# Kernel tuning notes

Hardware: AMD Instinct MI355X
Metric: run time of the kernel (lower is better)

## Reference

```python
import jax, jax.numpy as jnp
import numpy as np

N = 32768      # total nodes
E = 262144     # total edges (avg degree 8)
S = 128        # graph segments
B = 16         # batch entries
C = S // B     # segments per batch entry
NF, NC = 90, 36
OP, OD = 120, 64
D0, DX, GIN, GH = 190, 380, 256, 512


def setup_inputs() -> dict:
    key = jax.random.key(0)
    ks = jax.random.split(key, 16)
    rn = lambda k, shape, s=0.02: jax.random.normal(k, shape, jnp.float32) * s
    return {
        "node_features": jax.random.normal(ks[0], (N, NF), jnp.float32),
        "node_config_features": jax.random.normal(ks[1], (N, NC), jnp.float32),
        "emb_table": rn(ks[2], (OP, OD), 1.0),
        "w1": rn(ks[3], (DX, D0)), "b1": jnp.zeros((DX,), jnp.float32),
        "g1": jnp.ones((DX,), jnp.float32), "be1": jnp.zeros((DX,), jnp.float32),
        "w2": rn(ks[4], (GIN, DX)), "b2": jnp.zeros((GIN,), jnp.float32),
        "g2": jnp.ones((GIN,), jnp.float32), "be2": jnp.zeros((GIN,), jnp.float32),
        "wl1": rn(ks[5], (GH, GIN)), "bl1": jnp.zeros((GH,), jnp.float32), "wr1": rn(ks[6], (GH, GIN)),
        "wl2": rn(ks[7], (GH, GH)), "bl2": jnp.zeros((GH,), jnp.float32), "wr2": rn(ks[8], (GH, GH)),
        "wl3": rn(ks[9], (GH, GH)), "bl3": jnp.zeros((GH,), jnp.float32), "wr3": rn(ks[10], (GH, GH)),
        "wc": rn(ks[11], (1, GH)), "bc": jnp.zeros((1,), jnp.float32),
        "node_ops": jax.random.randint(ks[12], (N,), 0, OP),
        "edges": jax.random.randint(ks[13], (2, E), 0, N),
        # cumulative end indices, equal-size segments; batches = segment -> batch entry
        "node_separation": (jnp.arange(S, dtype=jnp.int32) + 1) * (N // S),
        "batches": jnp.repeat(jnp.arange(B, dtype=jnp.int32), C),
    }


def _leaky(x):
    return jnp.where(x >= 0, x, 0.01 * x)


def _graphwise_ln(x, seg_id, counts, gamma, beta):
    # per-graph-segment mean/var over all nodes and features, per-feature affine
    D = x.shape[1]
    s = jax.ops.segment_sum(jnp.sum(x, -1), seg_id, num_segments=S)
    ss = jax.ops.segment_sum(jnp.sum(x * x, -1), seg_id, num_segments=S)
    cnt = counts.astype(x.dtype) * D
    mean = s / cnt
    var = ss / cnt - mean * mean
    inv = jax.lax.rsqrt(var + 1e-5)
    return (x - mean[seg_id, None]) * inv[seg_id, None] * gamma + beta


def _pairnorm(x):
    # PyG PairNorm, scale=1: center over nodes, divide by sqrt(mean row norm^2)
    xc = x - jnp.mean(x, axis=0, keepdims=True)
    denom = 1e-5 + jnp.sqrt(jnp.mean(jnp.sum(xc * xc, -1)))
    return xc / denom


def _sage(x, src, dst, inv_deg, wl, bl, wr):
    # SAGEConv(mean): lin_l(mean_neighbors) + lin_r(x)
    agg = jax.ops.segment_sum(x[src], dst, num_segments=N) * inv_deg[:, None]
    return agg @ wl.T + bl + x @ wr.T


def reference(node_features, node_config_features, emb_table, w1, b1, g1, be1,
              w2, b2, g2, be2, wl1, bl1, wr1, wl2, bl2, wr2, wl3, bl3, wr3,
              wc, bc, node_ops, edges, node_separation, batches):
    seg_id = jnp.searchsorted(node_separation, jnp.arange(N), side="right")
    counts = jnp.diff(node_separation, prepend=0)
    src, dst = edges[0], edges[1]
    deg = jax.ops.segment_sum(jnp.ones((E,), jnp.float32), dst, num_segments=N)
    inv_deg = 1.0 / jnp.maximum(deg, 1.0)

    x = jnp.concatenate([node_features, node_config_features, emb_table[node_ops]], axis=1)
    # node_features_mlp: Linear -> LeakyReLU -> GLN -> Linear -> LeakyReLU -> GLN
    x = _graphwise_ln(_leaky(x @ w1.T + b1), seg_id, counts, g1, be1)
    x = _graphwise_ln(_leaky(x @ w2.T + b2), seg_id, counts, g2, be2)
    # GraphSAGE: 3 layers, PairNorm + ReLU after all but the last
    x = jax.nn.relu(_pairnorm(_sage(x, src, dst, inv_deg, wl1, bl1, wr1)))
    x = jax.nn.relu(_pairnorm(_sage(x, src, dst, inv_deg, wl2, bl2, wr2)))
    x = _sage(x, src, dst, inv_deg, wl3, bl3, wr3)
    # ragged per-segment sum pooling (replaces the python loop) -> [S, GH]
    seg_sums = jax.ops.segment_sum(x, seg_id, num_segments=S)
    # batches = repeat(arange(B), C) and segments are in order -> reshape groups
    agg = seg_sums.reshape(B, C, GH)
    out = agg @ wc.T + bc  # [B, C, 1]
    return jnp.squeeze(out, 2)
```

## Files before the change

kernel.cpp:

```cpp
#include <hip/hip_runtime.h>
#include <hip/hip_bf16.h>

#define NN   32768
#define EE   262144
#define SS   128
#define NF_  90
#define NC_  36
#define OD_  64
#define D0_  190
#define DX_  380
#define GIN_ 256
#define GH_  512

typedef __attribute__((ext_vector_type(8))) short  s8v;
typedef __attribute__((ext_vector_type(4))) float  f4v;

typedef const __attribute__((address_space(1))) void* gas_ptr;
typedef __attribute__((address_space(3))) void*       las_ptr;

__device__ __forceinline__ float bf2f(unsigned u) {
  return __uint_as_float(u << 16);
}
__device__ __forceinline__ unsigned short f2bf(float f) {
  unsigned u = __float_as_uint(f);
  u += 0x7FFFu + ((u >> 16) & 1u);
  return (unsigned short)(u >> 16);
}
__device__ __forceinline__ unsigned pack2(float a, float b) {
  return ((unsigned)f2bf(b) << 16) | (unsigned)f2bf(a);
}

__global__ void deg_count(const int* __restrict__ dst, int* __restrict__ deg) {
  int e = blockIdx.x * 256 + threadIdx.x;
  if (e < EE) atomicAdd(&deg[dst[e]], 1);
}

__global__ __launch_bounds__(256) void blk_sum_k(const int* __restrict__ deg,
                                                 int* __restrict__ bsum) {
  __shared__ int buf[256];
  int tid = threadIdx.x;
  buf[tid] = deg[blockIdx.x * 256 + tid];
  __syncthreads();
  for (int off = 128; off > 0; off >>= 1) {
    if (tid < off) buf[tid] += buf[tid + off];
    __syncthreads();
  }
  if (tid == 0) bsum[blockIdx.x] = buf[0];
}

__global__ __launch_bounds__(128) void blk_scan_k(const int* __restrict__ bsum,
                                                  int* __restrict__ boff) {
  __shared__ int buf[128];
  int tid = threadIdx.x;
  int v = bsum[tid];
  buf[tid] = v;
  __syncthreads();
  for (int d = 1; d < 128; d <<= 1) {
    int t = (tid >= d) ? buf[tid - d] : 0;
    __syncthreads();
    if (tid >= d) buf[tid] += t;
    __syncthreads();
  }
  boff[tid] = buf[tid] - v;
}

__global__ __launch_bounds__(256) void offsets_k(const int* __restrict__ deg,
                                                 const int* __restrict__ boff,
                                                 int* __restrict__ offsets,
                                                 float* __restrict__ inv_deg) {
  __shared__ int buf[256];
  int tid = threadIdx.x;
  int i = blockIdx.x * 256 + tid;
  int v = deg[i];
  buf[tid] = v;
  __syncthreads();
  for (int d = 1; d < 256; d <<= 1) {
    int t = (tid >= d) ? buf[tid - d] : 0;
    __syncthreads();
    if (tid >= d) buf[tid] += t;
    __syncthreads();
  }
  offsets[i] = boff[blockIdx.x] + buf[tid] - v;
  inv_deg[i] = 1.0f / fmaxf((float)v, 1.0f);
  if (i == 0) offsets[NN] = EE;
}

__global__ void bucket_k(const int* __restrict__ src, const int* __restrict__ dst,
                         const int* __restrict__ offsets, int* __restrict__ cursor,
                         int* __restrict__ srcs) {
  int e = blockIdx.x * 256 + threadIdx.x;
  if (e < EE) {
    int d = dst[e];
    int pos = offsets[d] + atomicAdd(&cursor[d], 1);
    srcs[pos] = src[e];
  }
}

#define CW1  73728
#define CW2  172032
#define CWL1 303104
#define CWR1 434176
#define CWL2 696320
#define CWR2 958464
#define CWL3 1220608
#define CWR3 1482752

__global__ __launch_bounds__(256) void prep_all(
    const float* __restrict__ nf, const float* __restrict__ ncf,
    const float* __restrict__ emb, const int* __restrict__ ops,
    const float* __restrict__ w1, const float* __restrict__ w2,
    const float* __restrict__ wl1, const float* __restrict__ wr1,
    const float* __restrict__ wl2, const float* __restrict__ wr2,
    const float* __restrict__ wl3, const float* __restrict__ wr3,
    unsigned short* __restrict__ w1b, unsigned short* __restrict__ w2b,
    unsigned short* __restrict__ wl1b, unsigned short* __restrict__ wr1b,
    unsigned short* __restrict__ wl2b, unsigned short* __restrict__ wr2b,
    unsigned short* __restrict__ wl3b, unsigned short* __restrict__ wr3b,
    unsigned short* __restrict__ x0,
    float* __restrict__ stat_all, float* __restrict__ outp,
    const float* __restrict__ bc)
{
  const int T = 4096 * 256;
  int gidx = blockIdx.x * 256 + threadIdx.x;
  for (int i = gidx; i < 2560; i += T) stat_all[i] = 0.0f;
  if (gidx < SS) outp[gidx] = bc[0];
  for (int i = gidx; i < CWR3; i += T) {
    if (i < CW1) {
      int r = i / 192, c = i - r * 192;
      w1b[i] = f2bf((r < DX_ && c < D0_) ? w1[r * D0_ + c] : 0.0f);
    } else if (i < CW2) {
      int j = i - CW1;
      int r = j / 384, c = j - r * 384;
      w2b[j] = f2bf((c < DX_) ? w2[r * DX_ + c] : 0.0f);
    } else if (i < CWL1) { int j = i - CW2;  wl1b[j] = f2bf(wl1[j]); }
    else if (i < CWR1)   { int j = i - CWL1; wr1b[j] = f2bf(wr1[j]); }
    else if (i < CWL2)   { int j = i - CWR1; wl2b[j] = f2bf(wl2[j]); }
    else if (i < CWR2)   { int j = i - CWL2; wr2b[j] = f2bf(wr2[j]); }
    else if (i < CWL3)   { int j = i - CWR2; wl3b[j] = f2bf(wl3[j]); }
    else                 { int j = i - CWL3; wr3b[j] = f2bf(wr3[j]); }
  }
  for (int i = gidx; i < NN * 192; i += T) {
    int n = i / 192;
    int c = i - n * 192;
    float v;
    if (c < NF_)            v = nf[n * NF_ + c];
    else if (c < NF_ + NC_) v = ncf[n * NC_ + (c - NF_)];
    else if (c < D0_)       v = emb[ops[n] * OD_ + (c - (NF_ + NC_))];
    else                    v = 0.0f;
    x0[i] = f2bf(v);
  }
}

__device__ __forceinline__ void stage_tile_async(const unsigned short* __restrict__ G, int ld,
                                                 int base_row, int k0,
                                                 unsigned short* __restrict__ lds, int tid) {
#pragma unroll
  for (int i = 0; i < 2; ++i) {
    int c = tid + i * 256;
    int row = c & 127;
    int off = c >> 7;
    const unsigned short* src = G + (size_t)(base_row + row) * ld + k0 + off * 8;
    unsigned short* dst = lds + off * 1024 + row * 8;
    __builtin_amdgcn_global_load_lds((gas_ptr)(const void*)src, (las_ptr)(void*)dst,
                                     16, 0, 0);
  }
}

__global__ __launch_bounds__(256) void mfma_gemm2(
    const unsigned short* __restrict__ A1, int lda1,
    const unsigned short* __restrict__ B1, int ldb1, int K1,
    const unsigned short* __restrict__ A2, int lda2,
    const unsigned short* __restrict__ B2, int ldb2, int K2,
    const float* __restrict__ bias,
    float* __restrict__ C, int ldc, int Nreal, int mode, int swz,
    float* __restrict__ st0, float* __restrict__ st1,
    const float* __restrict__ wcp, float* __restrict__ outp)
{
  __shared__ unsigned short As[4096];
  __shared__ unsigned short Bs[4096];
  int tid = threadIdx.x;
  int lane = tid & 63;
  int w = tid >> 6;
  int wm = (w & 1) * 64;
  int wn = (w >> 1) * 64;
  int bm, bn;
  if (swz) {
    int L = blockIdx.x;
    int xcd = L & 7;
    int s = L >> 3;
    bn = (s & 3) * 128;
    bm = ((s >> 2) * 8 + xcd) * 128;
  } else {
    bm = blockIdx.y * 128;
    bn = blockIdx.x * 128;
  }
  int quad = lane >> 4;
  int r16 = lane & 15;

  f4v acc[4][4] = {};

#pragma unroll 1
  for (int ph = 0; ph < 2; ++ph) {
    const unsigned short* A = ph ? A2 : A1;
    const unsigned short* B = ph ? B2 : B1;
    int lda = ph ? lda2 : lda1;
    int ldb = ph ? ldb2 : ldb1;
    int K = ph ? K2 : K1;
    for (int k0 = 0; k0 < K; k0 += 32) {
      stage_tile_async(A, lda, bm, k0, As, tid);
      stage_tile_async(B, ldb, bn, k0, Bs, tid);
      __syncthreads();
      s8v af[4], bfr[4];
#pragma unroll
      for (int mi = 0; mi < 4; ++mi)
        af[mi] = *(const s8v*)&As[quad * 1024 + (wm + mi * 16 + r16) * 8];
#pragma unroll
      for (int ni = 0; ni < 4; ++ni)
        bfr[ni] = *(const s8v*)&Bs[quad * 1024 + (wn + ni * 16 + r16) * 8];
#pragma unroll
      for (int mi = 0; mi < 4; ++mi)
#pragma unroll
        for (int ni = 0; ni < 4; ++ni)
          acc[mi][ni] = __builtin_amdgcn_mfma_f32_16x16x32_bf16(
              af[mi], bfr[ni], acc[mi][ni], 0, 0, 0);
      __syncthreads();
    }
  }

  float* red = (float*)As;
  float* cs  = (float*)Bs;
  float* css = ((float*)Bs) + 128;

  int seg = bm >> 8;

  if (mode == 1) {
    float lsum = 0.0f, lssq = 0.0f;
#pragma unroll
    for (int mi = 0; mi < 4; ++mi) {
      int gm = bm + wm + mi * 16 + quad * 4;
#pragma unroll
      for (int ni = 0; ni < 4; ++ni) {
        int gn = bn + wn + ni * 16 + r16;
        if (gn < Nreal) {
          float bv = bias[gn];
#pragma unroll
          for (int r = 0; r < 4; ++r) {
            float v = acc[mi][ni][r] + bv;
            v = (v >= 0.0f) ? v : 0.01f * v;
            C[(size_t)(gm + r) * ldc + gn] = v;
            lsum += v;
            lssq += v * v;
          }
        }
      }
    }
    red[tid] = lsum;
    __syncthreads();
    for (int off = 128; off > 0; off >>= 1) {
      if (tid < off) red[tid] += red[tid + off];
      __syncthreads();
    }
    if (tid == 0) atomicAdd(&st0[seg], red[0]);
    __syncthreads();
    red[tid] = lssq;
    __syncthreads();
    for (int off = 128; off > 0; off >>= 1) {
      if (tid < off) red[tid] += red[tid + off];
      __syncthreads();
    }
    if (tid == 0) atomicAdd(&st1[seg], red[0]);
  } else if (mode == 2) {
    if (tid < 128) { cs[tid] = 0.0f; css[tid] = 0.0f; }
    __syncthreads();
#pragma unroll
    for (int ni = 0; ni < 4; ++ni) {
      int col = wn + ni * 16 + r16;
      int gn = bn + col;
      float bv = bias[gn];
      float psum = 0.0f, pssq = 0.0f;
#pragma unroll
      for (int mi = 0; mi < 4; ++mi) {
        int gm = bm + wm + mi * 16 + quad * 4;
#pragma unroll
        for (int r = 0; r < 4; ++r) {
          float v = acc[mi][ni][r] + bv;
          C[(size_t)(gm + r) * ldc + gn] = v;
          psum += v;
          pssq += v * v;
        }
      }
      atomicAdd(&cs[col], psum);
      atomicAdd(&css[col], pssq);
    }
    __syncthreads();
    if (tid < 128) {
      atomicAdd(&st0[bn + tid], cs[tid]);
      atomicAdd(&st1[bn + tid], css[tid]);
    }
  } else {
    float part = 0.0f;
#pragma unroll
    for (int ni = 0; ni < 4; ++ni) {
      int gn = bn + wn + ni * 16 + r16;
      float bv = bias[gn];
      float wv = wcp[gn];
      float colsum = 0.0f;
#pragma unroll
      for (int mi = 0; mi < 4; ++mi)
#pragma unroll
        for (int r = 0; r < 4; ++r)
          colsum += acc[mi][ni][r] + bv;
      part += colsum * wv;
    }
    red[tid] = part;
    __syncthreads();
    for (int off = 128; off > 0; off >>= 1) {
      if (tid < off) red[tid] += red[tid + off];
      __syncthreads();
    }
    if (tid == 0) atomicAdd(&outp[seg], red[0]);
  }
}

__global__ __launch_bounds__(256) void gln_apply_bf16(
    const float* __restrict__ x, int ld, int D, int Dp,
    const float* __restrict__ seg_sum, const float* __restrict__ seg_ssq,
    const float* __restrict__ g, const float* __restrict__ be,
    unsigned short* __restrict__ out) {
  int r = blockIdx.x;
  int s = r >> 8;
  float cnt = 256.0f * (float)D;
  float m = seg_sum[s] / cnt;
  float var = seg_ssq[s] / cnt - m * m;
  float inv = rsqrtf(var + 1e-5f);
  const float* row = x + (size_t)r * ld;
  unsigned short* orow = out + (size_t)r * Dp;
  for (int c = threadIdx.x; c < Dp; c += 256) {
    float v = (c < D) ? ((row[c] - m) * inv * g[c] + be[c]) : 0.0f;
    orow[c] = f2bf(v);
  }
}

__global__ __launch_bounds__(256) void aggregate8(const unsigned short* __restrict__ x,
                                                  int L8,
                                                  unsigned short* __restrict__ agg,
                                                  const int* __restrict__ offsets,
                                                  const int* __restrict__ srcs,
                                                  const float* __restrict__ inv_deg) {
  int tid = threadIdx.x;
  int n = (blockIdx.x << (8 - L8)) + (tid >> L8);
  int f8 = tid & ((1 << L8) - 1);
  int start = offsets[n], end = offsets[n + 1];
  float wgt = inv_deg[n];
  const uint4* xb = (const uint4*)x;
  float a0 = 0, a1 = 0, a2 = 0, a3 = 0, a4 = 0, a5 = 0, a6 = 0, a7 = 0;
  for (int e = start; e < end; ++e) {
    uint4 v = xb[((size_t)srcs[e] << L8) + f8];
    a0 += bf2f(v.x & 0xffffu); a1 += bf2f(v.x >> 16);
    a2 += bf2f(v.y & 0xffffu); a3 += bf2f(v.y >> 16);
    a4 += bf2f(v.z & 0xffffu); a5 += bf2f(v.z >> 16);
    a6 += bf2f(v.w & 0xffffu); a7 += bf2f(v.w >> 16);
  }
  uint4 o;
  o.x = pack2(a0 * wgt, a1 * wgt);
  o.y = pack2(a2 * wgt, a3 * wgt);
  o.z = pack2(a4 * wgt, a5 * wgt);
  o.w = pack2(a6 * wgt, a7 * wgt);
  ((uint4*)agg)[((size_t)n << L8) + f8] = o;
}

__global__ __launch_bounds__(512) void pn_finalize(const float* __restrict__ colsum,
                                                   const float* __restrict__ colssq,
                                                   float* __restrict__ mu,
                                                   float* __restrict__ invd) {
  int f = threadIdx.x;
  float m = colsum[f] / (float)NN;
  mu[f] = m;
  float t = colssq[f] / (float)NN - m * m;
  __shared__ float buf[512];
  buf[f] = t;
  __syncthreads();
  for (int off = 256; off > 0; off >>= 1) {
    if (f < off) buf[f] += buf[f + off];
    __syncthreads();
  }
  if (f == 0) invd[0] = 1.0f / (1e-5f + sqrtf(fmaxf(buf[0], 0.0f)));
}

__global__ __launch_bounds__(128) void pn_apply_v(const float* __restrict__ y,
                                                  const float* __restrict__ mu,
                                                  const float* __restrict__ invd,
                                                  unsigned short* __restrict__ xb) {
  int r = blockIdx.x;
  int f4 = threadIdx.x;
  float id = invd[0];
  float4 v = ((const float4*)(y + (size_t)r * GH_))[f4];
  float4 m = ((const float4*)mu)[f4];
  float v0 = fmaxf((v.x - m.x) * id, 0.0f);
  float v1 = fmaxf((v.y - m.y) * id, 0.0f);
  float v2 = fmaxf((v.z - m.z) * id, 0.0f);
  float v3 = fmaxf((v.w - m.w) * id, 0.0f);
  uint2 o;
  o.x = pack2(v0, v1);
  o.y = pack2(v2, v3);
  ((uint2*)(xb + (size_t)r * GH_))[f4] = o;
}

extern "C" void kernel_launch(void* const* d_in, const int* in_sizes, int n_in,
                              void* d_out, int out_size, void* d_ws, size_t ws_size,
                              hipStream_t stream) {
  const float* node_features = (const float*)d_in[0];
  const float* node_config   = (const float*)d_in[1];
  const float* emb_table     = (const float*)d_in[2];
  const float* w1  = (const float*)d_in[3];
  const float* b1  = (const float*)d_in[4];
  const float* g1  = (const float*)d_in[5];
  const float* be1 = (const float*)d_in[6];
  const float* w2  = (const float*)d_in[7];
  const float* b2  = (const float*)d_in[8];
  const float* g2  = (const float*)d_in[9];
  const float* be2 = (const float*)d_in[10];
  const float* wl1 = (const float*)d_in[11];
  const float* bl1 = (const float*)d_in[12];
  const float* wr1 = (const float*)d_in[13];
  const float* wl2 = (const float*)d_in[14];
  const float* bl2 = (const float*)d_in[15];
  const float* wr2 = (const float*)d_in[16];
  const float* wl3 = (const float*)d_in[17];
  const float* bl3 = (const float*)d_in[18];
  const float* wr3 = (const float*)d_in[19];
  const float* wc  = (const float*)d_in[20];
  const float* bc  = (const float*)d_in[21];
  const int* node_ops = (const int*)d_in[22];
  const int* edges    = (const int*)d_in[23];
  float* out = (float*)d_out;

  char* ws = (char*)d_ws;
  size_t off = 0;
  auto alloc = [&](size_t bytes) -> void* {
    void* p = ws + off;
    off += (bytes + 255) & ~(size_t)255;
    return p;
  };

  int*   deg_i   = (int*)alloc(NN * 4);
  int*   cursor  = (int*)alloc(NN * 4);
  int*   offsets = (int*)alloc((NN + 1) * 4);
  int*   srcs    = (int*)alloc(EE * 4);
  int*   bsum    = (int*)alloc(SS * 4);
  int*   boff    = (int*)alloc(SS * 4);
  float* inv_deg = (float*)alloc(NN * 4);
  float* stat_all= (float*)alloc(2560 * 4);
  float* mu      = (float*)alloc(512 * 4);
  float* invd    = (float*)alloc(256);
  unsigned short* w1b  = (unsigned short*)alloc((size_t)384 * 192 * 2);
  unsigned short* w2b  = (unsigned short*)alloc((size_t)256 * 384 * 2);
  unsigned short* wl1b = (unsigned short*)alloc((size_t)512 * 256 * 2);
  unsigned short* wr1b = (unsigned short*)alloc((size_t)512 * 256 * 2);
  unsigned short* wl2b = (unsigned short*)alloc((size_t)512 * 512 * 2);
  unsigned short* wr2b = (unsigned short*)alloc((size_t)512 * 512 * 2);
  unsigned short* wl3b = (unsigned short*)alloc((size_t)512 * 512 * 2);
  unsigned short* wr3b = (unsigned short*)alloc((size_t)512 * 512 * 2);
  float*          Y    = (float*)alloc((size_t)NN * 512 * 4);
  unsigned short* BF1  = (unsigned short*)alloc((size_t)NN * 512 * 2);
  unsigned short* BF2  = (unsigned short*)alloc((size_t)NN * 512 * 2);
  unsigned short* BF3  = (unsigned short*)alloc((size_t)NN * 512 * 2);

  const int* esrc = edges;
  const int* edst = edges + EE;

  float* gln1s = stat_all;       float* gln1q = stat_all + 128;
  float* gln2s = stat_all + 256; float* gln2q = stat_all + 384;
  float* pn1s  = stat_all + 512; float* pn1q  = stat_all + 1024;
  float* pn2s  = stat_all + 1536; float* pn2q = stat_all + 2048;

  hipMemsetAsync(deg_i, 0, (size_t)NN * 4 * 2, stream);

  deg_count<<<EE / 256, 256, 0, stream>>>(edst, deg_i);
  blk_sum_k<<<NN / 256, 256, 0, stream>>>(deg_i, bsum);
  blk_scan_k<<<1, 128, 0, stream>>>(bsum, boff);
  offsets_k<<<NN / 256, 256, 0, stream>>>(deg_i, boff, offsets, inv_deg);
  bucket_k<<<EE / 256, 256, 0, stream>>>(esrc, edst, offsets, cursor, srcs);

  prep_all<<<4096, 256, 0, stream>>>(node_features, node_config, emb_table, node_ops,
                                     w1, w2, wl1, wr1, wl2, wr2, wl3, wr3,
                                     w1b, w2b, wl1b, wr1b, wl2b, wr2b, wl3b, wr3b,
                                     BF1, stat_all, out, bc);

  {
    dim3 g(3, 256);
    mfma_gemm2<<<g, 256, 0, stream>>>(BF1, 192, w1b, 192, 192,
                                      nullptr, 0, nullptr, 0, 0,
                                      b1, Y, 384, DX_, 1, 0,
                                      gln1s, gln1q, nullptr, nullptr);
  }
  gln_apply_bf16<<<NN, 256, 0, stream>>>(Y, 384, DX_, 384, gln1s, gln1q, g1, be1, BF2);

  {
    dim3 g(2, 256);
    mfma_gemm2<<<g, 256, 0, stream>>>(BF2, 384, w2b, 384, 384,
                                      nullptr, 0, nullptr, 0, 0,
                                      b2, Y, 256, GIN_, 1, 0,
                                      gln2s, gln2q, nullptr, nullptr);
  }
  gln_apply_bf16<<<NN, 256, 0, stream>>>(Y, 256, GIN_, 256, gln2s, gln2q, g2, be2, BF3);

  aggregate8<<<NN / 8, 256, 0, stream>>>(BF3, 5, BF1, offsets, srcs, inv_deg);
  mfma_gemm2<<<1024, 256, 0, stream>>>(BF1, 256, wl1b, 256, 256,
                                       BF3, 256, wr1b, 256, 256,
                                       bl1, Y, 512, GH_, 2, 1,
                                       pn1s, pn1q, nullptr, nullptr);
  pn_finalize<<<1, 512, 0, stream>>>(pn1s, pn1q, mu, invd);
  pn_apply_v<<<NN, 128, 0, stream>>>(Y, mu, invd, BF2);

  aggregate8<<<NN / 4, 256, 0, stream>>>(BF2, 6, BF1, offsets, srcs, inv_deg);
  mfma_gemm2<<<1024, 256, 0, stream>>>(BF1, 512, wl2b, 512, 512,
                                       BF2, 512, wr2b, 512, 512,
                                       bl2, Y, 512, GH_, 2, 1,
                                       pn2s, pn2q, nullptr, nullptr);
  pn_finalize<<<1, 512, 0, stream>>>(pn2s, pn2q, mu, invd);
  pn_apply_v<<<NN, 128, 0, stream>>>(Y, mu, invd, BF3);

  aggregate8<<<NN / 4, 256, 0, stream>>>(BF3, 6, BF1, offsets, srcs, inv_deg);
  mfma_gemm2<<<1024, 256, 0, stream>>>(BF1, 512, wl3b, 512, 512,
                                       BF3, 512, wr3b, 512, 512,
                                       bl3, nullptr, 512, GH_, 3, 1,
                                       nullptr, nullptr, wc, out);
}
```

Measured before the change: 601.6 us.

## Concatenate SAGE weights and activations into single-K GEMM with 64-wide K tiles

Stores the aggregated neighbour features and the self features side by side in one bf16 buffer, and packs wl|wr into one concatenated weight. Each SAGE layer then becomes one GEMM with doubled K instead of a two-phase GEMM. The GEMM K step grows from 32 to 64 with twice the LDS, which halves the barriers per output. The aggregation loop is also unrolled by two edges. The cost is a larger strided activation layout and more shared memory per block, which may lower occupancy.

```diff
diff --git a/kernel.cpp b/kernel.cpp
--- a/kernel.cpp
+++ b/kernel.cpp
@@ -96,14 +96,11 @@
   }
 }
 
-#define CW1  73728
-#define CW2  172032
-#define CWL1 303104
-#define CWR1 434176
-#define CWL2 696320
-#define CWR2 958464
-#define CWL3 1220608
-#define CWR3 1482752
+#define P1 73728
+#define P2 172032
+#define P3 434176
+#define P4 958464
+#define P5 1482752
 
 __global__ __launch_bounds__(256) void prep_all(
     const float* __restrict__ nf, const float* __restrict__ ncf,
@@ -113,9 +110,8 @@
     const float* __restrict__ wl2, const float* __restrict__ wr2,
     const float* __restrict__ wl3, const float* __restrict__ wr3,
     unsigned short* __restrict__ w1b, unsigned short* __restrict__ w2b,
-    unsigned short* __restrict__ wl1b, unsigned short* __restrict__ wr1b,
-    unsigned short* __restrict__ wl2b, unsigned short* __restrict__ wr2b,
-    unsigned short* __restrict__ wl3b, unsigned short* __restrict__ wr3b,
+    unsigned short* __restrict__ wc1, unsigned short* __restrict__ wc2,
+    unsigned short* __restrict__ wc3,
     unsigned short* __restrict__ x0,
     float* __restrict__ stat_all, float* __restrict__ outp,
     const float* __restrict__ bc)
@@ -124,20 +120,27 @@
   int gidx = blockIdx.x * 256 + threadIdx.x;
   for (int i = gidx; i < 2560; i += T) stat_all[i] = 0.0f;
   if (gidx < SS) outp[gidx] = bc[0];
-  for (int i = gidx; i < CWR3; i += T) {
-    if (i < CW1) {
+  for (int i = gidx; i < P5; i += T) {
+    if (i < P1) {
       int r = i / 192, c = i - r * 192;
       w1b[i] = f2bf((r < DX_ && c < D0_) ? w1[r * D0_ + c] : 0.0f);
-    } else if (i < CW2) {
-      int j = i - CW1;
+    } else if (i < P2) {
+      int j = i - P1;
       int r = j / 384, c = j - r * 384;
       w2b[j] = f2bf((c < DX_) ? w2[r * DX_ + c] : 0.0f);
-    } else if (i < CWL1) { int j = i - CW2;  wl1b[j] = f2bf(wl1[j]); }
-    else if (i < CWR1)   { int j = i - CWL1; wr1b[j] = f2bf(wr1[j]); }
-    else if (i < CWL2)   { int j = i - CWR1; wl2b[j] = f2bf(wl2[j]); }
-    else if (i < CWR2)   { int j = i - CWL2; wr2b[j] = f2bf(wr2[j]); }
-    else if (i < CWL3)   { int j = i - CWR2; wl3b[j] = f2bf(wl3[j]); }
-    else                 { int j = i - CWL3; wr3b[j] = f2bf(wr3[j]); }
+    } else if (i < P3) {
+      int j = i - P2;
+      int r = j >> 9, c = j & 511;
+      wc1[j] = f2bf((c < 256) ? wl1[r * 256 + c] : wr1[r * 256 + (c - 256)]);
+    } else if (i < P4) {
+      int j = i - P3;
+      int r = j >> 10, c = j & 1023;
+      wc2[j] = f2bf((c < 512) ? wl2[r * 512 + c] : wr2[r * 512 + (c - 512)]);
+    } else {
+      int j = i - P4;
+      int r = j >> 10, c = j & 1023;
+      wc3[j] = f2bf((c < 512) ? wl3[r * 512 + c] : wr3[r * 512 + (c - 512)]);
+    }
   }
   for (int i = gidx; i < NN * 192; i += T) {
     int n = i / 192;
@@ -151,33 +154,31 @@
   }
 }
 
-__device__ __forceinline__ void stage_tile_async(const unsigned short* __restrict__ G, int ld,
-                                                 int base_row, int k0,
-                                                 unsigned short* __restrict__ lds, int tid) {
-#pragma unroll
-  for (int i = 0; i < 2; ++i) {
+__device__ __forceinline__ void stage64(const unsigned short* __restrict__ G, int ld,
+                                        int base_row, int k0,
+                                        unsigned short* __restrict__ lds, int tid) {
+#pragma unroll
+  for (int i = 0; i < 4; ++i) {
     int c = tid + i * 256;
     int row = c & 127;
-    int off = c >> 7;
-    const unsigned short* src = G + (size_t)(base_row + row) * ld + k0 + off * 8;
-    unsigned short* dst = lds + off * 1024 + row * 8;
+    int koff = c >> 7;
+    const unsigned short* src = G + (size_t)(base_row + row) * ld + k0 + koff * 8;
+    unsigned short* dst = lds + koff * 1024 + row * 8;
     __builtin_amdgcn_global_load_lds((gas_ptr)(const void*)src, (las_ptr)(void*)dst,
                                      16, 0, 0);
   }
 }
 
-__global__ __launch_bounds__(256) void mfma_gemm2(
-    const unsigned short* __restrict__ A1, int lda1,
-    const unsigned short* __restrict__ B1, int ldb1, int K1,
-    const unsigned short* __restrict__ A2, int lda2,
-    const unsigned short* __restrict__ B2, int ldb2, int K2,
+__global__ __launch_bounds__(256) void mfma_gemm(
+    const unsigned short* __restrict__ A, int lda,
+    const unsigned short* __restrict__ B, int ldb, int K,
     const float* __restrict__ bias,
     float* __restrict__ C, int ldc, int Nreal, int mode, int swz,
     float* __restrict__ st0, float* __restrict__ st1,
     const float* __restrict__ wcp, float* __restrict__ outp)
 {
-  __shared__ unsigned short As[4096];
-  __shared__ unsigned short Bs[4096];
+  __shared__ unsigned short As[8192];
+  __shared__ unsigned short Bs[8192];
   int tid = threadIdx.x;
   int lane = tid & 63;
   int w = tid >> 6;
@@ -199,32 +200,27 @@
 
   f4v acc[4][4] = {};
 
-#pragma unroll 1
-  for (int ph = 0; ph < 2; ++ph) {
-    const unsigned short* A = ph ? A2 : A1;
-    const unsigned short* B = ph ? B2 : B1;
-    int lda = ph ? lda2 : lda1;
-    int ldb = ph ? ldb2 : ldb1;
-    int K = ph ? K2 : K1;
-    for (int k0 = 0; k0 < K; k0 += 32) {
-      stage_tile_async(A, lda, bm, k0, As, tid);
-      stage_tile_async(B, ldb, bn, k0, Bs, tid);
-      __syncthreads();
+  for (int k0 = 0; k0 < K; k0 += 64) {
+    stage64(A, lda, bm, k0, As, tid);
+    stage64(B, ldb, bn, k0, Bs, tid);
+    __syncthreads();
+#pragma unroll
+    for (int s = 0; s < 2; ++s) {
       s8v af[4], bfr[4];
 #pragma unroll
       for (int mi = 0; mi < 4; ++mi)
-        af[mi] = *(const s8v*)&As[quad * 1024 + (wm + mi * 16 + r16) * 8];
+        af[mi] = *(const s8v*)&As[(s * 4 + quad) * 1024 + (wm + mi * 16 + r16) * 8];
 #pragma unroll
       for (int ni = 0; ni < 4; ++ni)
-        bfr[ni] = *(const s8v*)&Bs[quad * 1024 + (wn + ni * 16 + r16) * 8];
+        bfr[ni] = *(const s8v*)&Bs[(s * 4 + quad) * 1024 + (wn + ni * 16 + r16) * 8];
 #pragma unroll
       for (int mi = 0; mi < 4; ++mi)
 #pragma unroll
         for (int ni = 0; ni < 4; ++ni)
           acc[mi][ni] = __builtin_amdgcn_mfma_f32_16x16x32_bf16(
               af[mi], bfr[ni], acc[mi][ni], 0, 0, 0);
-      __syncthreads();
-    }
+    }
+    __syncthreads();
   }
 
   float* red = (float*)As;
@@ -326,7 +322,7 @@
     const float* __restrict__ x, int ld, int D, int Dp,
     const float* __restrict__ seg_sum, const float* __restrict__ seg_ssq,
     const float* __restrict__ g, const float* __restrict__ be,
-    unsigned short* __restrict__ out) {
+    unsigned short* __restrict__ out, int ldo, int co) {
   int r = blockIdx.x;
   int s = r >> 8;
   float cnt = 256.0f * (float)D;
@@ -334,28 +330,40 @@
   float var = seg_ssq[s] / cnt - m * m;
   float inv = rsqrtf(var + 1e-5f);
   const float* row = x + (size_t)r * ld;
-  unsigned short* orow = out + (size_t)r * Dp;
+  unsigned short* orow = out + (size_t)r * ldo + co;
   for (int c = threadIdx.x; c < Dp; c += 256) {
     float v = (c < D) ? ((row[c] - m) * inv * g[c] + be[c]) : 0.0f;
     orow[c] = f2bf(v);
   }
 }
 
-__global__ __launch_bounds__(256) void aggregate8(const unsigned short* __restrict__ x,
-                                                  int L8,
-                                                  unsigned short* __restrict__ agg,
-                                                  const int* __restrict__ offsets,
-                                                  const int* __restrict__ srcs,
-                                                  const float* __restrict__ inv_deg) {
+__global__ __launch_bounds__(256) void aggregate8(
+    const unsigned short* __restrict__ xs, int ldu4, int cb4, int cba4, int L8,
+    unsigned short* __restrict__ aggs,
+    const int* __restrict__ offsets, const int* __restrict__ srcs,
+    const float* __restrict__ inv_deg) {
   int tid = threadIdx.x;
   int n = (blockIdx.x << (8 - L8)) + (tid >> L8);
   int f8 = tid & ((1 << L8) - 1);
   int start = offsets[n], end = offsets[n + 1];
   float wgt = inv_deg[n];
-  const uint4* xb = (const uint4*)x;
+  const uint4* xb = (const uint4*)xs;
   float a0 = 0, a1 = 0, a2 = 0, a3 = 0, a4 = 0, a5 = 0, a6 = 0, a7 = 0;
-  for (int e = start; e < end; ++e) {
-    uint4 v = xb[((size_t)srcs[e] << L8) + f8];
+  int e = start;
+  for (; e + 2 <= end; e += 2) {
+    uint4 v = xb[(size_t)srcs[e] * ldu4 + cb4 + f8];
+    uint4 u = xb[(size_t)srcs[e + 1] * ldu4 + cb4 + f8];
+    a0 += bf2f(v.x & 0xffffu); a1 += bf2f(v.x >> 16);
+    a2 += bf2f(v.y & 0xffffu); a3 += bf2f(v.y >> 16);
+    a4 += bf2f(v.z & 0xffffu); a5 += bf2f(v.z >> 16);
+    a6 += bf2f(v.w & 0xffffu); a7 += bf2f(v.w >> 16);
+    a0 += bf2f(u.x & 0xffffu); a1 += bf2f(u.x >> 16);
+    a2 += bf2f(u.y & 0xffffu); a3 += bf2f(u.y >> 16);
+    a4 += bf2f(u.z & 0xffffu); a5 += bf2f(u.z >> 16);
+    a6 += bf2f(u.w & 0xffffu); a7 += bf2f(u.w >> 16);
+  }
+  if (e < end) {
+    uint4 v = xb[(size_t)srcs[e] * ldu4 + cb4 + f8];
     a0 += bf2f(v.x & 0xffffu); a1 += bf2f(v.x >> 16);
     a2 += bf2f(v.y & 0xffffu); a3 += bf2f(v.y >> 16);
     a4 += bf2f(v.z & 0xffffu); a5 += bf2f(v.z >> 16);
@@ -366,7 +374,7 @@
   o.y = pack2(a2 * wgt, a3 * wgt);
   o.z = pack2(a4 * wgt, a5 * wgt);
   o.w = pack2(a6 * wgt, a7 * wgt);
-  ((uint4*)agg)[((size_t)n << L8) + f8] = o;
+  ((uint4*)aggs)[(size_t)n * ldu4 + cba4 + f8] = o;
 }
 
 __global__ __launch_bounds__(512) void pn_finalize(const float* __restrict__ colsum,
@@ -387,12 +395,14 @@
   if (f == 0) invd[0] = 1.0f / (1e-5f + sqrtf(fmaxf(buf[0], 0.0f)));
 }
 
-__global__ __launch_bounds__(128) void pn_apply_v(const float* __restrict__ y,
+__global__ __launch_bounds__(256) void pn_apply_v(const float* __restrict__ y,
                                                   const float* __restrict__ mu,
                                                   const float* __restrict__ invd,
-                                                  unsigned short* __restrict__ xb) {
-  int r = blockIdx.x;
-  int f4 = threadIdx.x;
+                                                  unsigned short* __restrict__ xb,
+                                                  int ldou2, int cou2) {
+  int t = threadIdx.x;
+  int r = blockIdx.x * 2 + (t >> 7);
+  int f4 = t & 127;
   float id = invd[0];
   float4 v = ((const float4*)(y + (size_t)r * GH_))[f4];
   float4 m = ((const float4*)mu)[f4];
@@ -403,7 +413,7 @@
   uint2 o;
   o.x = pack2(v0, v1);
   o.y = pack2(v2, v3);
-  ((uint2*)(xb + (size_t)r * GH_))[f4] = o;
+  ((uint2*)xb)[(size_t)r * ldou2 + cou2 + f4] = o;
 }
 
 extern "C" void kernel_launch(void* const* d_in, const int* in_sizes, int n_in,
@@ -453,26 +463,24 @@
   float* stat_all= (float*)alloc(2560 * 4);
   float* mu      = (float*)alloc(512 * 4);
   float* invd    = (float*)alloc(256);
-  unsigned short* w1b  = (unsigned short*)alloc((size_t)384 * 192 * 2);
-  unsigned short* w2b  = (unsigned short*)alloc((size_t)256 * 384 * 2);
-  unsigned short* wl1b = (unsigned short*)alloc((size_t)512 * 256 * 2);
-  unsigned short* wr1b = (unsigned short*)alloc((size_t)512 * 256 * 2);
-  unsigned short* wl2b = (unsigned short*)alloc((size_t)512 * 512 * 2);
-  unsigned short* wr2b = (unsigned short*)alloc((size_t)512 * 512 * 2);
-  unsigned short* wl3b = (unsigned short*)alloc((size_t)512 * 512 * 2);
-  unsigned short* wr3b = (unsigned short*)alloc((size_t)512 * 512 * 2);
-  float*          Y    = (float*)alloc((size_t)NN * 512 * 4);
-  unsigned short* BF1  = (unsigned short*)alloc((size_t)NN * 512 * 2);
-  unsigned short* BF2  = (unsigned short*)alloc((size_t)NN * 512 * 2);
-  unsigned short* BF3  = (unsigned short*)alloc((size_t)NN * 512 * 2);
+  unsigned short* w1b = (unsigned short*)alloc((size_t)384 * 192 * 2);
+  unsigned short* w2b = (unsigned short*)alloc((size_t)256 * 384 * 2);
+  unsigned short* wc1 = (unsigned short*)alloc((size_t)512 * 512 * 2);
+  unsigned short* wc2 = (unsigned short*)alloc((size_t)512 * 1024 * 2);
+  unsigned short* wc3 = (unsigned short*)alloc((size_t)512 * 1024 * 2);
+  unsigned short* X0  = (unsigned short*)alloc((size_t)NN * 192 * 2);
+  unsigned short* H1  = (unsigned short*)alloc((size_t)NN * 384 * 2);
+  unsigned short* XC1 = (unsigned short*)alloc((size_t)NN * 512 * 2);
+  unsigned short* XC2 = (unsigned short*)alloc((size_t)NN * 1024 * 2);
+  float*          Y   = (float*)alloc((size_t)NN * 512 * 4);
 
   const int* esrc = edges;
   const int* edst = edges + EE;
 
-  float* gln1s = stat_all;       float* gln1q = stat_all + 128;
-  float* gln2s = stat_all + 256; float* gln2q = stat_all + 384;
-  float* pn1s  = stat_all + 512; float* pn1q  = stat_all + 1024;
-  float* pn2s  = stat_all + 1536; float* pn2q = stat_all + 2048;
+  float* gln1s = stat_all;        float* gln1q = stat_all + 128;
+  float* gln2s = stat_all + 256;  float* gln2q = stat_all + 384;
+  float* pn1s  = stat_all + 512;  float* pn1q  = stat_all + 1024;
+  float* pn2s  = stat_all + 1536; float* pn2q  = stat_all + 2048;
 
   hipMemsetAsync(deg_i, 0, (size_t)NN * 4 * 2, stream);
 
@@ -484,46 +492,46 @@
 
   prep_all<<<4096, 256, 0, stream>>>(node_features, node_config, emb_table, node_ops,
                                      w1, w2, wl1, wr1, wl2, wr2, wl3, wr3,
-                                     w1b, w2b, wl1b, wr1b, wl2b, wr2b, wl3b, wr3b,
-                                     BF1, stat_all, out, bc);
+                                     w1b, w2b, wc1, wc2, wc3,
+                                     X0, stat_all, out, bc);
 
   {
     dim3 g(3, 256);
-    mfma_gemm2<<<g, 256, 0, stream>>>(BF1, 192, w1b, 192, 192,
-                                      nullptr, 0, nullptr, 0, 0,
-                                      b1, Y, 384, DX_, 1, 0,
-                                      gln1s, gln1q, nullptr, nullptr);
-  }
-  gln_apply_bf16<<<NN, 256, 0, stream>>>(Y, 384, DX_, 384, gln1s, gln1q, g1, be1, BF2);
+    mfma_gemm<<<g, 256, 0, stream>>>(X0, 192, w1b, 192, 192,
+                                     b1, Y, 384, DX_, 1, 0,
+                                     gln1s, gln1q, nullptr, nullptr);
+  }
+  gln_apply_bf16<<<NN, 256, 0, stream>>>(Y, 384, DX_, 384, gln1s, gln1q, g1, be1,
+                                         H1, 384, 0);
 
   {
     dim3 g(2, 256);
-    mfma_gemm2<<<g, 256, 0, stream>>>(BF2, 384, w2b, 384, 384,
-                                      nullptr, 0, nullptr, 0, 0,
-                                      b2, Y, 256, GIN_, 1, 0,
-                                      gln2s, gln2q, nullptr, nullptr);
-  }
-  gln_apply_bf16<<<NN, 256, 0, stream>>>(Y, 256, GIN_, 256, gln2s, gln2q, g2, be2, BF3);
-
-  aggregate8<<<NN / 8, 256, 0, stream>>>(BF3, 5, BF1, offsets, srcs, inv_deg);
-  mfma_gemm2<<<1024, 256, 0, stream>>>(BF1, 256, wl1b, 256, 256,
-                                       BF3, 256, wr1b, 256, 256,
-                                       bl1, Y, 512, GH_, 2, 1,
-                                       pn1s, pn1q, nullptr, nullptr);
+    mfma_gemm<<<g, 256, 0, stream>>>(H1, 384, w2b, 384, 384,
+                                     b2, Y, 256, GIN_, 1, 0,
+                                     gln2s, gln2q, nullptr, nullptr);
+  }
+  gln_apply_bf16<<<NN, 256, 0, stream>>>(Y, 256, GIN_, 256, gln2s, gln2q, g2, be2,
+                                         XC1, 512, 256);
+
+  aggregate8<<<NN / 8, 256, 0, stream>>>(XC1, 64, 32, 0, 5, XC1,
+                                         offsets, srcs, inv_deg);
+  mfma_gemm<<<1024, 256, 0, stream>>>(XC1, 512, wc1, 512, 512,
+                                      bl1, Y, 512, GH_, 2, 1,
+                                      pn1s, pn1q, nullptr, nullptr);
   pn_finalize<<<1, 512, 0, stream>>>(pn1s, pn1q, mu, invd);
-  pn_apply_v<<<NN, 128, 0, stream>>>(Y, mu, invd, BF2);
-
-  aggregate8<<<NN / 4, 256, 0, stream>>>(BF2, 6, BF1, offsets, srcs, inv_deg);
-  mfma_gemm2<<<1024, 256, 0, stream>>>(BF1, 512, wl2b, 512, 512,
-                                       BF2, 512, wr2b, 512, 512,
-                                       bl2, Y, 512, GH_, 2, 1,
-                                       pn2s, pn2q, nullptr, nullptr);
+  pn_apply_v<<<NN / 2, 256, 0, stream>>>(Y, mu, invd, XC2, 256, 128);
+
+  aggregate8<<<NN / 4, 256, 0, stream>>>(XC2, 128, 64, 0, 6, XC2,
+                                         offsets, srcs, inv_deg);
+  mfma_gemm<<<1024, 256, 0, stream>>>(XC2, 1024, wc2, 1024, 1024,
+                                      bl2, Y, 512, GH_, 2, 1,
+                                      pn2s, pn2q, nullptr, nullptr);
   pn_finalize<<<1, 512, 0, stream>>>(pn2s, pn2q, mu, invd);
-  pn_apply_v<<<NN, 128, 0, stream>>>(Y, mu, invd, BF3);
-
-  aggregate8<<<NN / 4, 256, 0, stream>>>(BF3, 6, BF1, offsets, srcs, inv_deg);
-  mfma_gemm2<<<1024, 256, 0, stream>>>(BF1, 512, wl3b, 512, 512,
-                                       BF3, 512, wr3b, 512, 512,
-                                       bl3, nullptr, 512, GH_, 3, 1,
-                                       nullptr, nullptr, wc, out);
-}
+  pn_apply_v<<<NN / 2, 256, 0, stream>>>(Y, mu, invd, XC2, 256, 128);
+
+  aggregate8<<<NN / 4, 256, 0, stream>>>(XC2, 128, 64, 0, 6, XC2,
+                                         offsets, srcs, inv_deg);
+  mfma_gemm<<<1024, 256, 0, stream>>>(XC2, 1024, wc3, 1024, 1024,
+                                      bl3, nullptr, 512, GH_, 3, 1,
+                                      nullptr, nullptr, wc, out);
+}
```

After: 584.6 us. -2.8%, faster.
